# Kernel optimization log

Measured on AMD Instinct MI355X. Metric: run time of the kernel, lower is better.

The kernel has to match this reference:

```python
import jax, jax.numpy as jnp
import numpy as np

D_MODEL = 512
N_HEADS = 8
ATTN_UNITS = 64
FF_UNITS = 2048
LN_EPS = 1e-3  # keras LayerNormalization default epsilon


def setup_inputs() -> dict:
    key = jax.random.key(0)
    ks = jax.random.split(key, 12)

    def glorot(k, shape):
        fan_in, fan_out = shape[-2], shape[-1]
        std = jnp.sqrt(2.0 / (fan_in + fan_out)).astype(jnp.float32)
        return jax.random.normal(k, shape, dtype=jnp.float32) * std

    x = jax.random.normal(ks[0], (8, 1024, D_MODEL), dtype=jnp.float32)
    qw = glorot(ks[1], (N_HEADS, D_MODEL, ATTN_UNITS))
    kw = glorot(ks[2], (N_HEADS, D_MODEL, ATTN_UNITS))
    vw = glorot(ks[3], (N_HEADS, D_MODEL, D_MODEL))
    lw = glorot(ks[4], (N_HEADS * D_MODEL, D_MODEL))
    w1 = glorot(ks[5], (D_MODEL, FF_UNITS))
    b1 = jax.random.normal(ks[6], (FF_UNITS,), dtype=jnp.float32) * 0.02
    w2 = glorot(ks[7], (FF_UNITS, D_MODEL))
    b2 = jax.random.normal(ks[8], (D_MODEL,), dtype=jnp.float32) * 0.02
    gamma1 = jnp.ones((D_MODEL,), dtype=jnp.float32)
    beta1 = jnp.zeros((D_MODEL,), dtype=jnp.float32)
    gamma2 = jnp.ones((D_MODEL,), dtype=jnp.float32)
    beta2 = jnp.zeros((D_MODEL,), dtype=jnp.float32)
    return {"x": x, "qw": qw, "kw": kw, "vw": vw, "lw": lw,
            "gamma1": gamma1, "beta1": beta1,
            "w1": w1, "b1": b1, "w2": w2, "b2": b2,
            "gamma2": gamma2, "beta2": beta2}


def _layer_norm(x, gamma, beta):
    mean = jnp.mean(x, axis=-1, keepdims=True)
    var = jnp.var(x, axis=-1, keepdims=True)
    return gamma * (x - mean) / jnp.sqrt(var + LN_EPS) + beta


def reference(x, qw, kw, vw, lw, gamma1, beta1, w1, b1, w2, b2, gamma2, beta2):
    B, S, D = x.shape
    H = qw.shape[0]
    scale = 1.0 / np.sqrt(D).astype(np.float32)

    # Batched per-head projections (replaces the Python loop over heads)
    q = jnp.einsum('bsd,hdu->bhsu', x, qw)      # [B,H,S,U]
    k = jnp.einsum('bsd,hdu->bhsu', x, kw)      # [B,H,S,U]
    v = jnp.einsum('bsd,hde->bhse', x, vw)      # [B,H,S,D]  (per-head value dim = D)

    scores = jnp.einsum('bhsu,bhtu->bhst', q, k) * scale  # [B,H,S,S]
    probs = jax.nn.softmax(scores, axis=-1)
    attn = jnp.einsum('bhst,bhte->bhse', probs, v)        # [B,H,S,D]

    # concat heads along feature axis, then output projection
    attn = attn.transpose(0, 2, 1, 3).reshape(B, S, H * D)
    mha = attn @ lw                                        # [B,S,D]

    # dropout in inference mode -> identity
    h = _layer_norm(x + mha, gamma1, beta1)

    ff = jax.nn.relu(h @ w1 + b1) @ w2 + b2
    out = _layer_norm(h + ff, gamma2, beta2)
    return out
```

## Files before the change

### kernel.cpp

```cpp
#include <hip/hip_runtime.h>
#include <stdint.h>


#define BM 128
#define BN 128
#define BK 64

typedef unsigned short u16;
typedef __attribute__((ext_vector_type(8))) short short8;
typedef __attribute__((ext_vector_type(4))) float f32x4;

__device__ __forceinline__ float bf2f(u16 b) {
  union { unsigned int u; float f; } c; c.u = ((unsigned int)b) << 16; return c.f;
}
__device__ __forceinline__ u16 f2bf(float f) {
  union { float f; unsigned int u; } c; c.f = f;
  unsigned int u = c.u;
  return (u16)((u + 0x7FFFu + ((u >> 16) & 1u)) >> 16);
}

#if __has_builtin(__builtin_amdgcn_exp2f)
#define EXP2(x) __builtin_amdgcn_exp2f(x)
#else
#define EXP2(x) exp2f(x)
#endif

#define GPTR(p) ((const __attribute__((address_space(1))) void*)(p))
#define LPTR(p) ((__attribute__((address_space(3))) void*)(p))

template<int EPI>
__launch_bounds__(256)
__global__ void gemm_bt(const u16* __restrict__ A, const u16* __restrict__ Bt,
                        void* __restrict__ Cv, const float* __restrict__ bias,
                        int K, int lda, int ldb, int ldc,
                        int batchInner,
                        long aOut, long aIn, long bOut, long bIn,
                        long cOut, long cIn, float scale, int swz)
{
  int bx = blockIdx.x, by = blockIdx.y;
  const int bz = blockIdx.z;
  if (swz == 1) {
    const int L = blockIdx.x + gridDim.x * blockIdx.y;
    const int xcd = L & 7;
    const int t = L >> 3;
    bx = t % gridDim.x;
    by = ((t / gridDim.x) << 3) | xcd;
  }

  const int zo = bz / batchInner;
  const int zi = bz - zo * batchInner;
  A  += zo * aOut + zi * aIn;
  Bt += zo * bOut + zi * bIn;
  const long cOff = zo * cOut + zi * cIn;

  const int m0 = by * BM;
  const int n0 = bx * BN;

  __shared__ u16 As[BM * BK];
  __shared__ u16 Bs[BN * BK];

  const int tid  = threadIdx.x;
  const int wave = tid >> 6;
  const int lane = tid & 63;
  const int wr = (wave >> 1) << 6;
  const int wc = (wave & 1) << 6;

  const int rsub = lane >> 3;
  const int kch  = (((lane & 7) ^ rsub) << 3);
  const int cb   = wave << 2;

  const u16* gA[4]; const u16* gB[4]; u16* lA[4]; u16* lB[4];
  #pragma unroll
  for (int j = 0; j < 4; ++j) {
    const int c = cb + j;
    gA[j] = A  + (long)(m0 + (c << 3) + rsub) * lda + kch;
    gB[j] = Bt + (long)(n0 + (c << 3) + rsub) * ldb + kch;
    lA[j] = As + c * 512;
    lB[j] = Bs + c * 512;
  }

  const int fr = lane & 15;
  const int kq = lane >> 4;
  const u16* pA[4][2]; const u16* pB[4][2];
  #pragma unroll
  for (int i = 0; i < 4; ++i)
    #pragma unroll
    for (int ks = 0; ks < 2; ++ks) {
      const int slot = (((ks << 2) | kq) ^ (fr & 7)) << 3;
      pA[i][ks] = As + (wr + (i << 4) + fr) * BK + slot;
      pB[i][ks] = Bs + (wc + (i << 4) + fr) * BK + slot;
    }

  f32x4 acc[4][4];
  #pragma unroll
  for (int i = 0; i < 4; ++i)
    #pragma unroll
    for (int j = 0; j < 4; ++j)
      acc[i][j] = (f32x4){0.f, 0.f, 0.f, 0.f};

  const int kIter = K >> 6;
  for (int kt = 0; kt < kIter; ++kt) {
    __syncthreads();
    #pragma unroll
    for (int j = 0; j < 4; ++j) {
      __builtin_amdgcn_global_load_lds(GPTR(gA[j]), LPTR(lA[j]), 16, 0, 0);
      __builtin_amdgcn_global_load_lds(GPTR(gB[j]), LPTR(lB[j]), 16, 0, 0);
    }
    #pragma unroll
    for (int j = 0; j < 4; ++j) { gA[j] += BK; gB[j] += BK; }
    __syncthreads();

    #pragma unroll
    for (int ks = 0; ks < 2; ++ks) {
      short8 af[4], bfv[4];
      #pragma unroll
      for (int i = 0; i < 4; ++i) af[i]  = *(const short8*)pA[i][ks];
      #pragma unroll
      for (int i = 0; i < 4; ++i) bfv[i] = *(const short8*)pB[i][ks];
      #pragma unroll
      for (int mi = 0; mi < 4; ++mi)
        #pragma unroll
        for (int ni = 0; ni < 4; ++ni)
          acc[mi][ni] = __builtin_amdgcn_mfma_f32_16x16x32_bf16(
              af[mi], bfv[ni], acc[mi][ni], 0, 0, 0);
    }
  }

  const int rq = (lane >> 4) << 2;
  #pragma unroll
  for (int mi = 0; mi < 4; ++mi) {
    #pragma unroll
    for (int ni = 0; ni < 4; ++ni) {
      const int col = n0 + wc + (ni << 4) + fr;
      float bv = 0.f;
      if (EPI == 3 || EPI == 4) bv = bias[col];
      #pragma unroll
      for (int r = 0; r < 4; ++r) {
        const int row = m0 + wr + (mi << 4) + rq + r;
        float v = acc[mi][ni][r];
        if (EPI == 1) v *= scale;
        v += bv;
        if (EPI == 3) v = fmaxf(v, 0.f);
        if (EPI == 0 || EPI == 1 || EPI == 3)
          ((u16*)Cv + cOff)[(long)row * ldc + col] = f2bf(v);
        else
          ((float*)Cv + cOff)[(long)row * ldc + col] = v;
      }
    }
  }
}

__launch_bounds__(256, 2)
__global__ void attn_fused(const u16* __restrict__ QKb, const u16* __restrict__ Vtb,
                           u16* __restrict__ attn)
{
  const int L = blockIdx.x + (blockIdx.y << 1) + (blockIdx.z << 4);
  const int xcd = L & 7;
  const int t0 = L >> 3;
  const int bh = ((t0 & 7) << 3) | xcd;
  const int r0_ = t0 >> 3;
  const int b = bh >> 3, h = bh & 7;
  const int q0 = (r0_ >> 1) << 7;
  const int e0 = (r0_ & 1) << 8;

  __shared__ u16 QP[8192];
  __shared__ u16 Kl[4096];
  __shared__ u16 Vl[16384];
  __shared__ __align__(16) float stats[128];

  const int tid  = threadIdx.x;
  const int wave = tid >> 6;
  const int lane = tid & 63;
  const int rsub = lane >> 3;
  const int kch  = ((lane & 7) ^ rsub) << 3;
  const int fr = lane & 15;
  const int kq = lane >> 4;
  const int rq = kq << 2;

  const u16* Qg = QKb + ((long)(b << 10) + q0) * 1024 + (h << 6);
  #pragma unroll
  for (int j = 0; j < 4; ++j) {
    const int c = (wave << 2) + j;
    __builtin_amdgcn_global_load_lds(
        GPTR(Qg + (long)((c << 3) + rsub) * 1024 + kch),
        LPTR(QP + c * 512), 16, 0, 0);
  }
  __syncthreads();

  short8 qb[2][2];
  #pragma unroll
  for (int ni = 0; ni < 2; ++ni)
    #pragma unroll
    for (int ks = 0; ks < 2; ++ks) {
      const int row = (wave << 5) + (ni << 4) + fr;
      const int phys = (((ks << 2) | kq) ^ (fr & 7)) << 3;
      qb[ni][ks] = *(const short8*)(QP + row * 64 + phys);
    }

  u16* Pl = QP;

  const u16* gK[2]; const u16* gV[8];
  #pragma unroll
  for (int j = 0; j < 2; ++j)
    gK[j] = QKb + ((long)(b << 10) + ((wave * 2 + j) << 3) + rsub) * 1024
                + 512 + (h << 6) + kch;
  #pragma unroll
  for (int j = 0; j < 8; ++j)
    gV[j] = Vtb + ((long)bh * 512 + e0 + ((wave * 8 + j) << 3) + rsub) * 1024 + kch;

  f32x4 o[8][4];
  #pragma unroll
  for (int qt = 0; qt < 8; ++qt)
    #pragma unroll
    for (int ni = 0; ni < 4; ++ni)
      o[qt][ni] = (f32x4){0.f, 0.f, 0.f, 0.f};
  float l_[2] = {0.f, 0.f};

  for (int tt = 0; tt < 16; ++tt) {
    __syncthreads();
    #pragma unroll
    for (int j = 0; j < 2; ++j)
      __builtin_amdgcn_global_load_lds(GPTR(gK[j]), LPTR(Kl + (wave * 2 + j) * 512), 16, 0, 0);
    #pragma unroll
    for (int j = 0; j < 8; ++j)
      __builtin_amdgcn_global_load_lds(GPTR(gV[j]), LPTR(Vl + (wave * 8 + j) * 512), 16, 0, 0);
    #pragma unroll
    for (int j = 0; j < 2; ++j) gK[j] += 64 * 1024;
    #pragma unroll
    for (int j = 0; j < 8; ++j) gV[j] += 64;
    __syncthreads();

    f32x4 st[4][2];
    #pragma unroll
    for (int mi = 0; mi < 4; ++mi)
      #pragma unroll
      for (int ni = 0; ni < 2; ++ni)
        st[mi][ni] = (f32x4){0.f, 0.f, 0.f, 0.f};
    #pragma unroll
    for (int ks = 0; ks < 2; ++ks) {
      const int phys = (((ks << 2) | kq) ^ (fr & 7)) << 3;
      short8 kf[4];
      #pragma unroll
      for (int mi = 0; mi < 4; ++mi)
        kf[mi] = *(const short8*)(Kl + ((mi << 4) + fr) * 64 + phys);
      #pragma unroll
      for (int mi = 0; mi < 4; ++mi)
        #pragma unroll
        for (int ni = 0; ni < 2; ++ni)
          st[mi][ni] = __builtin_amdgcn_mfma_f32_16x16x32_bf16(
              kf[mi], qb[ni][ks], st[mi][ni], 0, 0, 0);
    }

    #pragma unroll
    for (int ni = 0; ni < 2; ++ni) {
      const int qlocal = (ni << 4) + fr;
      u16* prow = Pl + ((wave << 5) + qlocal) * 64 + ((kq & 1) << 2);
      float rs = 0.f;
      #pragma unroll
      for (int mi = 0; mi < 4; ++mi) {
        const float p0 = EXP2(st[mi][ni][0]);
        const float p1 = EXP2(st[mi][ni][1]);
        const float p2 = EXP2(st[mi][ni][2]);
        const float p3 = EXP2(st[mi][ni][3]);
        rs += (p0 + p1) + (p2 + p3);
        const int chunk = ((((mi << 1) | (kq >> 1)) ^ (qlocal & 7)) << 3);
        uint2 pk;
        pk.x = (uint32_t)f2bf(p0) | ((uint32_t)f2bf(p1) << 16);
        pk.y = (uint32_t)f2bf(p2) | ((uint32_t)f2bf(p3) << 16);
        *(uint2*)(prow + chunk) = pk;
      }
      l_[ni] += rs;
    }

    __syncthreads();

    #pragma unroll
    for (int ks = 0; ks < 2; ++ks) {
      const int phys = (((ks << 2) | kq) ^ (fr & 7)) << 3;
      short8 vb[4];
      #pragma unroll
      for (int ni = 0; ni < 4; ++ni)
        vb[ni] = *(const short8*)(Vl + ((wave << 6) + (ni << 4) + fr) * 64 + phys);
      #pragma unroll
      for (int qt = 0; qt < 8; ++qt) {
        const short8 pa = *(const short8*)(Pl + ((qt << 4) + fr) * 64 + phys);
        #pragma unroll
        for (int ni = 0; ni < 4; ++ni)
          o[qt][ni] = __builtin_amdgcn_mfma_f32_16x16x32_bf16(
              pa, vb[ni], o[qt][ni], 0, 0, 0);
      }
    }
  }

  #pragma unroll
  for (int ni = 0; ni < 2; ++ni) {
    float s = l_[ni];
    s += __shfl_xor(s, 16);
    s += __shfl_xor(s, 32);
    l_[ni] = s;
  }
  if (kq == 0) {
    stats[(wave << 5) + fr]      = 1.f / l_[0];
    stats[(wave << 5) + 16 + fr] = 1.f / l_[1];
  }
  __syncthreads();

  #pragma unroll
  for (int qt = 0; qt < 8; ++qt) {
    const f32x4 il = *(const f32x4*)(stats + (qt << 4) + rq);
    #pragma unroll
    for (int ni = 0; ni < 4; ++ni) {
      const int col = (h << 9) + e0 + (wave << 6) + (ni << 4) + fr;
      #pragma unroll
      for (int r = 0; r < 4; ++r) {
        const long row = (long)(b << 10) + q0 + (qt << 4) + rq + r;
        attn[row * 4096 + col] = f2bf(o[qt][ni][r] * il[r]);
      }
    }
  }
}

__global__ void transpose_cast(const float* __restrict__ src, u16* __restrict__ dst,
                               int R, int C, long sBatch, long dBatch, float mul)
{
  __shared__ float tile[32][33];
  src += (long)blockIdx.z * sBatch;
  dst += (long)blockIdx.z * dBatch;
  const int c0 = blockIdx.x << 5, r0 = blockIdx.y << 5;
  const int tx = threadIdx.x, ty = threadIdx.y;
  #pragma unroll
  for (int i = 0; i < 32; i += 8) {
    int r = r0 + ty + i, c = c0 + tx;
    if (r < R && c < C) tile[ty + i][tx] = src[(long)r * C + c];
  }
  __syncthreads();
  #pragma unroll
  for (int i = 0; i < 32; i += 8) {
    int c = c0 + ty + i, r = r0 + tx;
    if (c < C && r < R) dst[(long)c * R + r] = f2bf(tile[tx][ty + i] * mul);
  }
}

__global__ void cast_bf16(const float* __restrict__ src, u16* __restrict__ dst, int n4)
{
  int t = blockIdx.x * blockDim.x + threadIdx.x;
  if (t < n4) {
    float4 v = ((const float4*)src)[t];
    uint2 o;
    o.x = (unsigned)f2bf(v.x) | ((unsigned)f2bf(v.y) << 16);
    o.y = (unsigned)f2bf(v.z) | ((unsigned)f2bf(v.w) << 16);
    ((uint2*)dst)[t] = o;
  }
}

__global__ void add_ln_red(const float* __restrict__ a, const float* __restrict__ P,
                           long pstride, int nsplit, const float* __restrict__ bias,
                           const float* __restrict__ gamma, const float* __restrict__ beta,
                           float* __restrict__ outF, u16* __restrict__ outB)
{
  const long row = blockIdx.x;
  const int tid = threadIdx.x;
  const int wave = tid >> 6, lane = tid & 63;
  float4 va = ((const float4*)(a + (row << 9)))[tid];
  float x0 = va.x, x1 = va.y, x2 = va.z, x3 = va.w;
  for (int sp = 0; sp < nsplit; ++sp) {
    float4 p = ((const float4*)(P + sp * pstride + (row << 9)))[tid];
    x0 += p.x; x1 += p.y; x2 += p.z; x3 += p.w;
  }
  if (bias) {
    float4 bv = ((const float4*)bias)[tid];
    x0 += bv.x; x1 += bv.y; x2 += bv.z; x3 += bv.w;
  }
  float s = x0 + x1 + x2 + x3;
  float q = x0*x0 + x1*x1 + x2*x2 + x3*x3;
  #pragma unroll
  for (int off = 32; off > 0; off >>= 1) {
    s += __shfl_xor(s, off);
    q += __shfl_xor(q, off);
  }
  __shared__ float red[4];
  if (lane == 0) { red[wave] = s; red[2 + wave] = q; }
  __syncthreads();
  s = red[0] + red[1]; q = red[2] + red[3];
  float mu  = s * (1.f / 512.f);
  float var = q * (1.f / 512.f) - mu * mu;
  float rstd = rsqrtf(var + 1e-3f);
  float4 g  = ((const float4*)gamma)[tid];
  float4 be = ((const float4*)beta)[tid];
  float o0 = g.x * (x0 - mu) * rstd + be.x;
  float o1 = g.y * (x1 - mu) * rstd + be.y;
  float o2 = g.z * (x2 - mu) * rstd + be.z;
  float o3 = g.w * (x3 - mu) * rstd + be.w;
  ((float4*)(outF + (row << 9)))[tid] = make_float4(o0, o1, o2, o3);
  if (outB) {
    uint2 o;
    o.x = (unsigned)f2bf(o0) | ((unsigned)f2bf(o1) << 16);
    o.y = (unsigned)f2bf(o2) | ((unsigned)f2bf(o3) << 16);
    ((uint2*)(outB + (row << 9)))[tid] = o;
  }
}

extern "C" void kernel_launch(void* const* d_in, const int* in_sizes, int n_in,
                              void* d_out, int out_size, void* d_ws, size_t ws_size,
                              hipStream_t stream)
{
  (void)in_sizes; (void)n_in; (void)out_size;
  const float* x      = (const float*)d_in[0];
  const float* qw     = (const float*)d_in[1];
  const float* kw     = (const float*)d_in[2];
  const float* vw     = (const float*)d_in[3];
  const float* lw     = (const float*)d_in[4];
  const float* gamma1 = (const float*)d_in[5];
  const float* beta1  = (const float*)d_in[6];
  const float* w1     = (const float*)d_in[7];
  const float* b1     = (const float*)d_in[8];
  const float* w2     = (const float*)d_in[9];
  const float* b2     = (const float*)d_in[10];
  const float* gamma2 = (const float*)d_in[11];
  const float* beta2  = (const float*)d_in[12];

  const int Bb = 8, S = 1024, D = 512, H = 8, F = 2048;
  const int N = Bb * S;
  const float qmul = 0.04419417382415922f * 1.4426950408889634f;

  char* w = (char*)d_ws;
  size_t off = 0;
  auto alloc = [&](size_t bytes) -> char* {
    char* p = w + off; off += (bytes + 255) & ~(size_t)255; return p;
  };
  u16* Xbf  = (u16*)alloc((size_t)N * D * 2);
  u16* WqkT = (u16*)alloc((size_t)2 * D * D * 2);
  u16* WvT  = (u16*)alloc((size_t)H * D * D * 2);
  u16* lwT  = (u16*)alloc((size_t)D * (H * D) * 2);
  u16* w1T  = (u16*)alloc((size_t)F * D * 2);
  u16* w2T  = (u16*)alloc((size_t)D * F * 2);
  char* qkArena = alloc((size_t)N * 2 * D * 2);
  char* bigArena = alloc((size_t)N * (H * D) * 2);
  const size_t fixedEnd = off;

  u16*   QKb  = (u16*)qkArena;
  u16*   attn = (u16*)bigArena;
  float* hbuf = (float*)bigArena;
  u16*   hbf  = (u16*)(bigArena + (size_t)N * D * 4);
  u16*   ff1  = (u16*)(bigArena + (size_t)N * D * 4 + (size_t)N * D * 2);

  u16*   Vtb = (u16*)(w + fixedEnd);
  const long pstride = (long)N * D;
  int SK = (ws_size - fixedEnd >= (size_t)4 * pstride * 4) ? 4 : 1;
  float* part = (float*)(w + fixedEnd);

  dim3 tb(32, 8);
  cast_bf16<<<dim3(N * D / 4 / 256), 256, 0, stream>>>(x, Xbf, N * D / 4);
  transpose_cast<<<dim3(2, 16, 8),  tb, 0, stream>>>(qw, WqkT, 512, 64, 32768, 32768, qmul);
  transpose_cast<<<dim3(2, 16, 8),  tb, 0, stream>>>(kw, WqkT + (size_t)D * D, 512, 64, 32768, 32768, 1.f);
  transpose_cast<<<dim3(16, 16, 8), tb, 0, stream>>>(vw, WvT, 512, 512, 262144, 262144, 1.f);
  transpose_cast<<<dim3(16, 128, 1),tb, 0, stream>>>(lw, lwT, 4096, 512, 0, 0, 1.f);
  transpose_cast<<<dim3(64, 16, 1), tb, 0, stream>>>(w1, w1T, 512, 2048, 0, 0, 1.f);
  transpose_cast<<<dim3(16, 64, 1), tb, 0, stream>>>(w2, w2T, 2048, 512, 0, 0, 1.f);

  gemm_bt<0><<<dim3(8, 64, 1), 256, 0, stream>>>(Xbf, WqkT, QKb, nullptr,
      512, 512, 512, 1024, 1, 0, 0, 0, 0, 0, 0, 0.f, 1);

  gemm_bt<0><<<dim3(8, 4, 64), 256, 0, stream>>>(WvT, Xbf, Vtb, nullptr,
      512, 512, 512, 1024, H,
      0, (long)D * D,
      (long)S * D, 0,
      (long)H * D * S, (long)D * S, 0.f, 0);

  attn_fused<<<dim3(2, 8, 64), 256, 0, stream>>>(QKb, Vtb, attn);

  gemm_bt<2><<<dim3(4, 64, SK), 256, 0, stream>>>(attn, lwT, part, nullptr,
      4096 / SK, 4096, 4096, 512, 1,
      4096 / SK, 0, 4096 / SK, 0, pstride, 0, 0.f, 1);

  add_ln_red<<<dim3(N), 128, 0, stream>>>(x, part, pstride, SK, nullptr,
                                          gamma1, beta1, hbuf, hbf);

  gemm_bt<3><<<dim3(16, 64, 1), 256, 0, stream>>>(hbf, w1T, ff1, b1,
      512, 512, 512, 2048, 1, 0, 0, 0, 0, 0, 0, 0.f, 1);

  gemm_bt<2><<<dim3(4, 64, SK), 256, 0, stream>>>(ff1, w2T, part, nullptr,
      2048 / SK, 2048, 2048, 512, 1,
      2048 / SK, 0, 2048 / SK, 0, pstride, 0, 0.f, 1);

  add_ln_red<<<dim3(N), 128, 0, stream>>>(hbuf, part, pstride, SK, b2,
                                          gamma2, beta2, (float*)d_out, nullptr);
}
```

Before: 404.8 us.

## Halve attention query tile and load Q/K fragments directly into registers

The fused attention kernel now processes 64 query rows per block instead of 128, doubling the grid and halving the output accumulator registers, with launch bounds raised to allow three blocks per CU. Q and K fragments are read straight from global memory into registers rather than staged through LDS, which shrinks shared memory. The aim is higher occupancy and more blocks in flight to hide latency. The cost is that each V tile is loaded twice as often across blocks, and K is fetched by every wave without LDS sharing.

```diff
diff --git a/kernel.cpp b/kernel.cpp
--- a/kernel.cpp
+++ b/kernel.cpp
@@ -150,23 +150,22 @@
   }
 }
 
-__launch_bounds__(256, 2)
+__launch_bounds__(256, 3)
 __global__ void attn_fused(const u16* __restrict__ QKb, const u16* __restrict__ Vtb,
                            u16* __restrict__ attn)
 {
-  const int L = blockIdx.x + (blockIdx.y << 1) + (blockIdx.z << 4);
+  const int L = blockIdx.x + (blockIdx.y << 1) + (blockIdx.z << 5);
   const int xcd = L & 7;
   const int t0 = L >> 3;
   const int bh = ((t0 & 7) << 3) | xcd;
   const int r0_ = t0 >> 3;
   const int b = bh >> 3, h = bh & 7;
-  const int q0 = (r0_ >> 1) << 7;
+  const int q0 = (r0_ >> 1) << 6;
   const int e0 = (r0_ & 1) << 8;
 
-  __shared__ u16 QP[8192];
-  __shared__ u16 Kl[4096];
+  __shared__ u16 Pl[4096];
   __shared__ u16 Vl[16384];
-  __shared__ __align__(16) float stats[128];
+  __shared__ __align__(16) float stats[64];
 
   const int tid  = threadIdx.x;
   const int wave = tid >> 6;
@@ -177,99 +176,73 @@
   const int kq = lane >> 4;
   const int rq = kq << 2;
 
-  const u16* Qg = QKb + ((long)(b << 10) + q0) * 1024 + (h << 6);
-  #pragma unroll
-  for (int j = 0; j < 4; ++j) {
-    const int c = (wave << 2) + j;
-    __builtin_amdgcn_global_load_lds(
-        GPTR(Qg + (long)((c << 3) + rsub) * 1024 + kch),
-        LPTR(QP + c * 512), 16, 0, 0);
-  }
-  __syncthreads();
-
-  short8 qb[2][2];
-  #pragma unroll
-  for (int ni = 0; ni < 2; ++ni)
-    #pragma unroll
-    for (int ks = 0; ks < 2; ++ks) {
-      const int row = (wave << 5) + (ni << 4) + fr;
-      const int phys = (((ks << 2) | kq) ^ (fr & 7)) << 3;
-      qb[ni][ks] = *(const short8*)(QP + row * 64 + phys);
-    }
-
-  u16* Pl = QP;
-
-  const u16* gK[2]; const u16* gV[8];
-  #pragma unroll
-  for (int j = 0; j < 2; ++j)
-    gK[j] = QKb + ((long)(b << 10) + ((wave * 2 + j) << 3) + rsub) * 1024
-                + 512 + (h << 6) + kch;
+  const u16* qptr = QKb + ((long)(b << 10) + q0 + (wave << 4) + fr) * 1024
+                        + (h << 6) + (kq << 3);
+  short8 qb[2];
+  qb[0] = *(const short8*)(qptr);
+  qb[1] = *(const short8*)(qptr + 32);
+
+  const u16* kptr = QKb + ((long)(b << 10) + fr) * 1024
+                        + 512 + (h << 6) + (kq << 3);
+
+  const u16* gV[8];
   #pragma unroll
   for (int j = 0; j < 8; ++j)
     gV[j] = Vtb + ((long)bh * 512 + e0 + ((wave * 8 + j) << 3) + rsub) * 1024 + kch;
 
-  f32x4 o[8][4];
-  #pragma unroll
-  for (int qt = 0; qt < 8; ++qt)
+  f32x4 o[4][4];
+  #pragma unroll
+  for (int qt = 0; qt < 4; ++qt)
     #pragma unroll
     for (int ni = 0; ni < 4; ++ni)
       o[qt][ni] = (f32x4){0.f, 0.f, 0.f, 0.f};
-  float l_[2] = {0.f, 0.f};
+  float l_ = 0.f;
 
   for (int tt = 0; tt < 16; ++tt) {
+    short8 kf[4][2];
+    #pragma unroll
+    for (int mi = 0; mi < 4; ++mi) {
+      const u16* kp = kptr + (long)((tt << 6) + (mi << 4)) * 1024;
+      kf[mi][0] = *(const short8*)(kp);
+      kf[mi][1] = *(const short8*)(kp + 32);
+    }
+
     __syncthreads();
-    #pragma unroll
-    for (int j = 0; j < 2; ++j)
-      __builtin_amdgcn_global_load_lds(GPTR(gK[j]), LPTR(Kl + (wave * 2 + j) * 512), 16, 0, 0);
     #pragma unroll
     for (int j = 0; j < 8; ++j)
       __builtin_amdgcn_global_load_lds(GPTR(gV[j]), LPTR(Vl + (wave * 8 + j) * 512), 16, 0, 0);
     #pragma unroll
-    for (int j = 0; j < 2; ++j) gK[j] += 64 * 1024;
-    #pragma unroll
     for (int j = 0; j < 8; ++j) gV[j] += 64;
     __syncthreads();
 
-    f32x4 st[4][2];
-    #pragma unroll
-    for (int mi = 0; mi < 4; ++mi)
-      #pragma unroll
-      for (int ni = 0; ni < 2; ++ni)
-        st[mi][ni] = (f32x4){0.f, 0.f, 0.f, 0.f};
-    #pragma unroll
-    for (int ks = 0; ks < 2; ++ks) {
-      const int phys = (((ks << 2) | kq) ^ (fr & 7)) << 3;
-      short8 kf[4];
+    f32x4 st[4];
+    #pragma unroll
+    for (int mi = 0; mi < 4; ++mi) st[mi] = (f32x4){0.f, 0.f, 0.f, 0.f};
+    #pragma unroll
+    for (int ks = 0; ks < 2; ++ks)
       #pragma unroll
       for (int mi = 0; mi < 4; ++mi)
-        kf[mi] = *(const short8*)(Kl + ((mi << 4) + fr) * 64 + phys);
-      #pragma unroll
-      for (int mi = 0; mi < 4; ++mi)
-        #pragma unroll
-        for (int ni = 0; ni < 2; ++ni)
-          st[mi][ni] = __builtin_amdgcn_mfma_f32_16x16x32_bf16(
-              kf[mi], qb[ni][ks], st[mi][ni], 0, 0, 0);
-    }
-
-    #pragma unroll
-    for (int ni = 0; ni < 2; ++ni) {
-      const int qlocal = (ni << 4) + fr;
-      u16* prow = Pl + ((wave << 5) + qlocal) * 64 + ((kq & 1) << 2);
+        st[mi] = __builtin_amdgcn_mfma_f32_16x16x32_bf16(
+            kf[mi][ks], qb[ks], st[mi], 0, 0, 0);
+
+    {
+      const int row = (wave << 4) + fr;
+      u16* prow = Pl + row * 64 + ((kq & 1) << 2);
       float rs = 0.f;
       #pragma unroll
       for (int mi = 0; mi < 4; ++mi) {
-        const float p0 = EXP2(st[mi][ni][0]);
-        const float p1 = EXP2(st[mi][ni][1]);
-        const float p2 = EXP2(st[mi][ni][2]);
-        const float p3 = EXP2(st[mi][ni][3]);
+        const float p0 = EXP2(st[mi][0]);
+        const float p1 = EXP2(st[mi][1]);
+        const float p2 = EXP2(st[mi][2]);
+        const float p3 = EXP2(st[mi][3]);
         rs += (p0 + p1) + (p2 + p3);
-        const int chunk = ((((mi << 1) | (kq >> 1)) ^ (qlocal & 7)) << 3);
+        const int chunk = ((((mi << 1) | (kq >> 1)) ^ (fr & 7)) << 3);
         uint2 pk;
         pk.x = (uint32_t)f2bf(p0) | ((uint32_t)f2bf(p1) << 16);
         pk.y = (uint32_t)f2bf(p2) | ((uint32_t)f2bf(p3) << 16);
         *(uint2*)(prow + chunk) = pk;
       }
-      l_[ni] += rs;
+      l_ += rs;
     }
 
     __syncthreads();
@@ -282,7 +255,7 @@
       for (int ni = 0; ni < 4; ++ni)
         vb[ni] = *(const short8*)(Vl + ((wave << 6) + (ni << 4) + fr) * 64 + phys);
       #pragma unroll
-      for (int qt = 0; qt < 8; ++qt) {
+      for (int qt = 0; qt < 4; ++qt) {
         const short8 pa = *(const short8*)(Pl + ((qt << 4) + fr) * 64 + phys);
         #pragma unroll
         for (int ni = 0; ni < 4; ++ni)
@@ -292,21 +265,16 @@
     }
   }
 
-  #pragma unroll
-  for (int ni = 0; ni < 2; ++ni) {
-    float s = l_[ni];
+  {
+    float s = l_;
     s += __shfl_xor(s, 16);
     s += __shfl_xor(s, 32);
-    l_[ni] = s;
-  }
-  if (kq == 0) {
-    stats[(wave << 5) + fr]      = 1.f / l_[0];
-    stats[(wave << 5) + 16 + fr] = 1.f / l_[1];
+    if (kq == 0) stats[(wave << 4) + fr] = 1.f / s;
   }
   __syncthreads();
 
   #pragma unroll
-  for (int qt = 0; qt < 8; ++qt) {
+  for (int qt = 0; qt < 4; ++qt) {
     const f32x4 il = *(const f32x4*)(stats + (qt << 4) + rq);
     #pragma unroll
     for (int ni = 0; ni < 4; ++ni) {
@@ -467,7 +435,7 @@
       (long)S * D, 0,
       (long)H * D * S, (long)D * S, 0.f, 0);
 
-  attn_fused<<<dim3(2, 8, 64), 256, 0, stream>>>(QKb, Vtb, attn);
+  attn_fused<<<dim3(2, 16, 64), 256, 0, stream>>>(QKb, Vtb, attn);
 
   gemm_bt<2><<<dim3(4, 64, SK), 256, 0, stream>>>(attn, lwT, part, nullptr,
       4096 / SK, 4096, 4096, 512, 1,
```

After: 498.8 us. 1.23x slower.
